# Optimization experiments

Measured on AMD Instinct MI355X. Metric: run time of the kernel, lower is better.

Reference implementation:

```python
import jax, jax.numpy as jnp
import numpy as np

R, B, F, C, NCLS = 32, 4096, 256, 4, 1000  # n_rules, batch, n_fea, n_channel, n_cls
K, PAD, POOL = 5, 1, 2                     # kernel_size, padding, pooling_size


def setup_inputs() -> dict:
    key = jax.random.key(0)
    ks = jax.random.split(key, 12)
    L0 = F + 2 * PAD - K + 1          # 254 after conv1
    L1 = L0 // POOL                   # 127 after avgpool1
    L2 = (L1 + 2 * PAD - K + 1) // POOL  # 62 after conv2+avgpool2
    att = C * L2                      # 248 (matches torch att_size formula)
    hid = att // 2                    # 124
    s = lambda k, shape: jax.random.normal(k, shape, dtype=jnp.float32) * 0.05
    return dict(
        data=jax.random.normal(ks[0], (B, F), dtype=jnp.float32),
        proto=s(ks[1], (R, F)),
        conv1_w=s(ks[2], (C, 1, K)), conv1_b=s(ks[3], (C,)),
        conv2_w=s(ks[4], (C, C, K)), conv2_b=s(ks[5], (C,)),
        fc1_w=s(ks[6], (att, hid)), fc1_b=s(ks[7], (hid,)),
        fc2_w=s(ks[8], (hid, 1)), fc2_b=s(ks[9], (1,)),
        consq_w=s(ks[10], (R, F, NCLS)), consq_b=s(ks[11], (R, NCLS)),
        is_train=0,
    )


def _conv1d(x, w, b):
    # x: [N, Cin, L], w: [Cout, Cin, K]
    out = jax.lax.conv_general_dilated(
        x, w, window_strides=(1,), padding=[(PAD, PAD)],
        dimension_numbers=('NCH', 'OIH', 'NCH'))
    return out + b[None, :, None]


def _avgpool2(x):
    # non-overlapping AvgPool1d(2), drops trailing remainder like torch
    L2 = x.shape[-1] // POOL
    return x[..., :L2 * POOL].reshape(x.shape[0], x.shape[1], L2, POOL).mean(-1)


def reference(data, proto, conv1_w, conv1_b, conv2_w, conv2_b,
              fc1_w, fc1_b, fc2_w, fc2_b, consq_w, consq_b, is_train):
    n_batch = data.shape[0]
    # data_diff: [R, B, F] -> shared gating net, fold rules into batch
    diff = (data[None, :, :] - proto[:, None, :]).reshape(R * n_batch, 1, F)
    h = _avgpool2(jax.nn.relu(_conv1d(diff, conv1_w, conv1_b)))
    h = _avgpool2(jax.nn.relu(_conv1d(h, conv2_w, conv2_b)))
    h = h.reshape(R * n_batch, -1)                       # [R*B, att]
    h = jax.nn.relu(h @ fc1_w + fc1_b)                   # [R*B, hid]
    fs_ini = jnp.tanh(h @ fc2_w + fc2_b)                 # [R*B, 1]
    fs_ini = fs_ini.reshape(R, n_batch).T                # cat(dim=1) -> [B, R]
    fs = jax.nn.softmax(fs_ini, axis=1)                  # softmax over rules
    # per-rule experts: grouped matmul [B,F] x [R,F,NCLS]
    expert = jnp.einsum('bf,rfc->rbc', data, consq_w) + consq_b[:, None, :]
    return jnp.einsum('br,rbc->bc', fs, expert)          # [B, NCLS]
```

## Files before the change

kernel.cpp:

```cpp
#include <hip/hip_runtime.h>
#include <hip/hip_bf16.h>

using bf16x8 = __attribute__((ext_vector_type(8))) short;
using f32x4  = __attribute__((ext_vector_type(4))) float;
using v2f    = __attribute__((ext_vector_type(2))) float;

__device__ __forceinline__ unsigned short f2bf_rne(float x) {
    unsigned u = __float_as_uint(x);
    u += 0x7fffu + ((u >> 16) & 1u);
    return (unsigned short)(u >> 16);
}

__device__ __forceinline__ void gload_lds16(const void* g, void* l) {
    __builtin_amdgcn_global_load_lds(
        (const __attribute__((address_space(1))) unsigned int*)g,
        (__attribute__((address_space(3))) unsigned int*)l, 16, 0, 0);
}

constexpr int KP = 8320;
constexpr int KROW = KP * 2;

constexpr size_t OFF_DT  = 0;
constexpr size_t OFF_Q1  = OFF_DT  + (size_t)260 * 4096 * 4;
constexpr size_t OFF_BT  = OFF_Q1  + (size_t)32 * 1024 * 4;
constexpr size_t OFF_C1P = OFF_BT;
constexpr size_t OFF_W1S = OFF_BT  + (size_t)1024 * KP * 2;
constexpr size_t OFF_FSI = OFF_W1S + (size_t)128 * 256 * 2;
constexpr size_t OFF_FS  = OFF_FSI + (size_t)32 * 4096 * 4;
constexpr size_t OFF_ASC = OFF_FS  + (size_t)32 * 4096 * 4;
constexpr size_t OFF_H2  = OFF_ASC;
constexpr size_t OFF_P1  = OFF_ASC + (size_t)4096 * KP * 2;

__global__ __launch_bounds__(256) void k_transpose(const float* __restrict__ data,
                                                   float* __restrict__ dTp) {
    __shared__ float tile[64][65];
    int bx = blockIdx.x & 63;
    int fx = blockIdx.x >> 6;
    int tx = threadIdx.x & 63, ty4 = threadIdx.x >> 6;
#pragma unroll
    for (int i = 0; i < 16; ++i) {
        int ty = ty4 * 16 + i;
        tile[ty][tx] = data[(bx * 64 + ty) * 256 + fx * 64 + tx];
    }
    __syncthreads();
#pragma unroll
    for (int i = 0; i < 16; ++i) {
        int ty = ty4 * 16 + i;
        dTp[(size_t)(fx * 64 + ty + 1) * 4096 + bx * 64 + tx] = tile[tx][ty];
    }
}

__global__ __launch_bounds__(256) void k_zrows(float* __restrict__ dTp) {
    int i = blockIdx.x * 256 + threadIdx.x;
    dTp[i] = 0.f;
    dTp[(size_t)257 * 4096 + i] = 0.f;
}

__global__ __launch_bounds__(256) void k_prep_proto(const float* __restrict__ proto,
                                                    const float* __restrict__ w1,
                                                    const float* __restrict__ b1,
                                                    float* __restrict__ q1p) {
    __shared__ float ps[256];
    __shared__ float w1s[20];
    int r = blockIdx.x, tid = threadIdx.x;
    ps[tid] = proto[r * 256 + tid];
    if (tid < 20) w1s[tid] = w1[tid];
    __syncthreads();
    if (tid < 254) {
#pragma unroll
        for (int c = 0; c < 4; ++c) {
            float s = -b1[c];
#pragma unroll
            for (int k = 0; k < 5; ++k) {
                int x = tid + k - 1;
                float xv = (x >= 0 && x < 256) ? ps[x] : 0.f;
                s += w1s[c * 5 + k] * xv;
            }
            q1p[r * 1024 + c * 256 + tid] = s;
        }
    }
}

__global__ __launch_bounds__(64) void k_prep_c1d(const float* __restrict__ dTp,
                                                 const float* __restrict__ w1,
                                                 float2* __restrict__ c1p) {
    int lane = threadIdx.x;
    int bg = blockIdx.x >> 3, ch = blockIdx.x & 7;
    int l0 = ch << 4;
    int nl = (ch == 7) ? 15 : 16;
    int b = (bg << 6) + lane;
    float w1r[20];
#pragma unroll
    for (int i = 0; i < 20; ++i) w1r[i] = w1[i];
    const float* dp = dTp + (size_t)(2 * l0) * 4096 + b;
    float d[6];
#pragma unroll
    for (int i = 0; i < 6; ++i) d[i] = dp[(size_t)i * 4096];
    dp += (size_t)6 * 4096;
    float2* outp = c1p + b;
    for (int li = 0; li < nl; ++li) {
        int l = l0 + li;
#pragma unroll
        for (int c = 0; c < 4; ++c) {
            float s0 = 0.f, s1 = 0.f;
#pragma unroll
            for (int k = 0; k < 5; ++k) {
                s0 += w1r[c * 5 + k] * d[k];
                s1 += w1r[c * 5 + k] * d[k + 1];
            }
            outp[(size_t)(c * 127 + l) * 4096] = make_float2(s0, s1);
        }
        d[0] = d[2]; d[1] = d[3]; d[2] = d[4]; d[3] = d[5];
        d[4] = dp[0];
        d[5] = dp[4096];
        dp += 8192;
    }
}

__global__ __launch_bounds__(256) void k_castB(const float* __restrict__ cw,
                                               const float* __restrict__ cb,
                                               unsigned short* __restrict__ BT) {
    __shared__ unsigned short L[64 * 137];
    int tid = threadIdx.x;
    int kt = blockIdx.x >> 3, ct = blockIdx.x & 7;
    int k0 = kt << 6, c0 = ct << 7;
#pragma unroll
    for (int i = 0; i < 32; ++i) {
        int flat = i * 256 + tid;
        int cl = flat & 127, kl = flat >> 7;
        int cg = c0 + cl;
        int kg = k0 + kl;
        float v = 0.f;
        if (cg < 1000) {
            if (kg < 8192) v = cw[(size_t)kg * 1000 + cg];
            else if (kg < 8224) v = cb[(size_t)(kg - 8192) * 1000 + cg];
        }
        L[kl * 137 + cl] = f2bf_rne(v);
    }
    __syncthreads();
#pragma unroll
    for (int i = 0; i < 4; ++i) {
        int task = i * 256 + tid;
        int kg = task & 7, cl = task >> 3;
        int base = kg * 8 * 137 + cl;
        unsigned x = (unsigned)L[base] | ((unsigned)L[base + 137] << 16);
        unsigned y = (unsigned)L[base + 2 * 137] | ((unsigned)L[base + 3 * 137] << 16);
        unsigned z = (unsigned)L[base + 4 * 137] | ((unsigned)L[base + 5 * 137] << 16);
        unsigned w = (unsigned)L[base + 6 * 137] | ((unsigned)L[base + 7 * 137] << 16);
        uint4 o; o.x = x; o.y = y; o.z = z; o.w = w;
        int cg = c0 + cl;
        size_t byte = (size_t)cg * KROW + (size_t)(kt << 7) + (size_t)((kg ^ (cg & 7)) << 4);
        *(uint4*)((char*)BT + byte) = o;
    }
}

__global__ __launch_bounds__(256) void k_castW(const float* __restrict__ fc1w,
                                               unsigned short* __restrict__ W1s) {
    int idx = blockIdx.x * 256 + threadIdx.x;
    int col = idx >> 8, k = idx & 255;
    float v = 0.f;
    if (col < 124 && k < 248) {
        int f = (k & 3) * 62 + (k >> 2);
        v = fc1w[f * 124 + col];
    }
    int byte = col * 512 + ((k >> 6) << 7) + ((((k >> 3) & 7) ^ (col & 7)) << 4) + ((k & 7) << 1);
    *(unsigned short*)((char*)W1s + byte) = f2bf_rne(v);
}

__global__ __launch_bounds__(64)
void k_conv2(const float2* __restrict__ c1p,
             const float* __restrict__ q1p,
             const float* __restrict__ w2,
             const float* __restrict__ b2,
             char* __restrict__ h2c) {
    __shared__ unsigned short T[64 * 72];

    int lane = threadIdx.x;
    int job = blockIdx.x;
    int jh = job & 1;
    int bc = (job >> 1) & 63;
    int r  = job >> 7;
    int b0 = bc << 6;
    int b = b0 + lane;
    int rb0 = r * 4096 + b0;
    int j2s = jh ? 32 : 0;
    int j2e = jh ? 62 : 32;

    float w2r[80];
#pragma unroll
    for (int i = 0; i < 80; ++i) w2r[i] = w2[i];
    v2f bb[4];
#pragma unroll
    for (int c = 0; c < 4; ++c) { float t = b2[c]; bb[c][0] = t; bb[c][1] = t; }

    const float* q1row = q1p + r * 1024;
    const float2* cpb = c1p + b;

    auto pooled = [&](int c, int l) -> float {
        float2 v = cpb[(size_t)(c * 127 + l) * 4096];
        float2 q = *(const float2*)(q1row + c * 256 + 2 * l);
        return 0.5f * (fmaxf(v.x - q.x, 0.f) + fmaxf(v.y - q.y, 0.f));
    };

    v2f P[4][5];
#pragma unroll
    for (int c = 0; c < 4; ++c) {
        float pv[6];
#pragma unroll
        for (int idx = 0; idx < 6; ++idx) {
            int l = 2 * j2s - 1 + idx;
            pv[idx] = (l < 0) ? 0.f : pooled(c, l);
        }
#pragma unroll
        for (int k = 0; k < 5; ++k) { P[c][k][0] = pv[k]; P[c][k][1] = pv[k + 1]; }
    }

#pragma unroll 2
    for (int j2 = j2s; j2 < j2e; ++j2) {
        v2f u[4];
#pragma unroll
        for (int c = 0; c < 4; ++c) u[c] = bb[c];
#pragma unroll
        for (int c = 0; c < 4; ++c)
#pragma unroll
            for (int ci = 0; ci < 4; ++ci)
#pragma unroll
                for (int k = 0; k < 5; ++k)
                    u[c] += P[ci][k] * w2r[(c * 4 + ci) * 5 + k];
        {
            float h0 = 0.5f * (fmaxf(u[0][0], 0.f) + fmaxf(u[0][1], 0.f));
            float h1 = 0.5f * (fmaxf(u[1][0], 0.f) + fmaxf(u[1][1], 0.f));
            float h2v = 0.5f * (fmaxf(u[2][0], 0.f) + fmaxf(u[2][1], 0.f));
            float h3 = 0.5f * (fmaxf(u[3][0], 0.f) + fmaxf(u[3][1], 0.f));
            uint2 vv;
            vv.x = (unsigned)f2bf_rne(h0) | ((unsigned)f2bf_rne(h1) << 16);
            vv.y = (unsigned)f2bf_rne(h2v) | ((unsigned)f2bf_rne(h3) << 16);
            *(uint2*)(T + lane * 72 + (j2 & 15) * 4) = vv;
        }
        if (j2 == 61) {
            uint4 z; z.x = z.y = z.z = z.w = 0u;
            *(uint4*)(T + lane * 72 + 56) = z;
        }
        if ((j2 & 15) == 15 || j2 == 61) {
            int chunk = j2 >> 4;
            int g = lane & 7;
#pragma unroll
            for (int i = 0; i < 8; ++i) {
                int sL = i * 8 + (lane >> 3);
                bf16x8 v = *(const bf16x8*)(T + sL * 72 + g * 8);
                int srow = rb0 + sL;
                size_t byte = (size_t)srow * 512 + (size_t)(chunk * 128) + (size_t)((g ^ (srow & 7)) << 4);
                *(bf16x8*)(h2c + byte) = v;
            }
        }
        if (j2 < j2e - 1) {
#pragma unroll
            for (int c = 0; c < 4; ++c) {
                float n0 = pooled(c, 2 * j2 + 5);
                float n1 = pooled(c, 2 * j2 + 6);
                v2f p4v = P[c][4];
                P[c][0] = P[c][2]; P[c][1] = P[c][3]; P[c][2] = p4v;
                v2f t3; t3[0] = p4v[1]; t3[1] = n0;
                v2f t4; t4[0] = n0;     t4[1] = n1;
                P[c][3] = t3; P[c][4] = t4;
            }
        }
    }
}

__global__ __launch_bounds__(256) void k_fc(const char* __restrict__ h2,
                                            const char* __restrict__ W1s,
                                            const float* __restrict__ fc1b,
                                            const float* __restrict__ fc2w,
                                            const float* __restrict__ fc2b,
                                            float* __restrict__ fsiniT) {
    int tid = threadIdx.x, lane = tid & 63, w = tid >> 6;
    int row0 = blockIdx.x * 128 + w * 32;
    int lr = lane & 15, g = lane >> 4, rxor = lr & 7;

    f32x4 acc[2][8] = {};

    const char* arow0 = h2 + (size_t)(row0 + lr) * 512;
    const char* arow1 = arow0 + 16 * 512;

    auto inrowf = [&](int ks) {
        return ((ks >> 1) << 7) + ((((ks * 4 + g) & 7) ^ rxor) << 4);
    };

    bf16x8 a0 = *(const bf16x8*)(arow0 + inrowf(0));
    bf16x8 a1 = *(const bf16x8*)(arow1 + inrowf(0));

#pragma unroll
    for (int ks = 0; ks < 8; ++ks) {
        int ir = inrowf(ks);
        bf16x8 bfr[8];
#pragma unroll
        for (int nf = 0; nf < 8; ++nf)
            bfr[nf] = *(const bf16x8*)(W1s + (nf * 16 + lr) * 512 + ir);
        bf16x8 an0 = a0, an1 = a1;
        if (ks < 7) {
            int ir2 = inrowf(ks + 1);
            an0 = *(const bf16x8*)(arow0 + ir2);
            an1 = *(const bf16x8*)(arow1 + ir2);
        }
#pragma unroll
        for (int nf = 0; nf < 8; ++nf) {
            acc[0][nf] = __builtin_amdgcn_mfma_f32_16x16x32_bf16(a0, bfr[nf], acc[0][nf], 0, 0, 0);
            acc[1][nf] = __builtin_amdgcn_mfma_f32_16x16x32_bf16(a1, bfr[nf], acc[1][nf], 0, 0, 0);
        }
        a0 = an0; a1 = an1;
    }

    float zp[2][4] = {};
#pragma unroll
    for (int nf = 0; nf < 8; ++nf) {
        int col = nf * 16 + lr;
        float b1v = (col < 124) ? fc1b[col] : 0.f;
        float w2v = (col < 124) ? fc2w[col] : 0.f;
#pragma unroll
        for (int mf = 0; mf < 2; ++mf)
#pragma unroll
            for (int q = 0; q < 4; ++q) {
                float h = fmaxf(acc[mf][nf][q] + b1v, 0.f);
                zp[mf][q] += h * w2v;
            }
    }
#pragma unroll
    for (int off = 1; off < 16; off <<= 1) {
#pragma unroll
        for (int mf = 0; mf < 2; ++mf)
#pragma unroll
            for (int q = 0; q < 4; ++q)
                zp[mf][q] += __shfl_xor(zp[mf][q], off, 64);
    }
    if (lr == 0) {
        float c2 = fc2b[0];
#pragma unroll
        for (int mf = 0; mf < 2; ++mf)
#pragma unroll
            for (int q = 0; q < 4; ++q) {
                int srow = row0 + mf * 16 + g * 4 + q;
                fsiniT[srow] = tanhf(zp[mf][q] + c2);
            }
    }
}

__global__ __launch_bounds__(256) void k_softmax(const float* __restrict__ fsiniT,
                                                 float* __restrict__ fsT) {
    int b = blockIdx.x * 256 + threadIdx.x;
    float v[32];
    float m = -1e30f;
#pragma unroll
    for (int r = 0; r < 32; ++r) { v[r] = fsiniT[r * 4096 + b]; m = fmaxf(m, v[r]); }
    float s = 0.f;
#pragma unroll
    for (int r = 0; r < 32; ++r) { v[r] = expf(v[r] - m); s += v[r]; }
    float inv = 1.f / s;
#pragma unroll
    for (int r = 0; r < 32; ++r) fsT[r * 4096 + b] = v[r] * inv;
}

__global__ __launch_bounds__(256) void k_scaleA(const float* __restrict__ data,
                                                const float* __restrict__ fsT,
                                                unsigned short* __restrict__ Asc) {
    int g = blockIdx.x * 256 + threadIdx.x;
    int b = g / 1040, kg = g - b * 1040;
    uint4 o;
    unsigned* op = (unsigned*)&o;
    if (kg < 1024) {
        int r = kg >> 5, f0 = (kg & 31) << 3;
        float fs = fsT[r * 4096 + b];
        const float4* dp = (const float4*)(data + b * 256 + f0);
        float4 v0 = dp[0], v1 = dp[1];
        float vals[8] = {v0.x, v0.y, v0.z, v0.w, v1.x, v1.y, v1.z, v1.w};
#pragma unroll
        for (int i = 0; i < 4; ++i) {
            unsigned lo = f2bf_rne(vals[2 * i] * fs);
            unsigned hi = f2bf_rne(vals[2 * i + 1] * fs);
            op[i] = lo | (hi << 16);
        }
    } else {
        int base = (kg - 1024) << 3;
        op[0] = op[1] = op[2] = op[3] = 0u;
        if (base < 32) {
#pragma unroll
            for (int i = 0; i < 4; ++i) {
                unsigned lo = f2bf_rne(fsT[(base + 2 * i) * 4096 + b]);
                unsigned hi = f2bf_rne(fsT[(base + 2 * i + 1) * 4096 + b]);
                op[i] = lo | (hi << 16);
            }
        }
    }
    size_t byte = (size_t)b * KROW + (size_t)((kg & ~7) << 4) + (size_t)(((kg & 7) ^ (b & 7)) << 4);
    *(uint4*)((char*)Asc + byte) = o;
}

__global__ __launch_bounds__(512) void k_gemm(const unsigned short* __restrict__ Asc,
                                              const unsigned short* __restrict__ BT,
                                              float* __restrict__ out,
                                              _Float16* __restrict__ part1) {
    __shared__ unsigned short As[2][8192];
    __shared__ unsigned short Bs[2][8192];
    int tid = threadIdx.x, lane = tid & 63, w = tid >> 6;
    int wm = w >> 2, wn = w & 3;
    int bid = blockIdx.x;
    int xcd = bid & 7, idx = bid >> 3;
    int mt = (xcd << 2) | (idx >> 4);
    int nt = (idx >> 1) & 7;
    int ks = idx & 1;
    int row0 = mt << 7, col0 = nt << 7;

    f32x4 acc[4][2] = {};

    const char* Ab = (const char*)Asc + (size_t)ks * (KP);
    const char* Bb = (const char*)BT + (size_t)ks * (KP);
    int flat0 = tid * 16, flat1 = tid * 16 + 8192;
    int rowl0 = flat0 >> 7, colB0 = flat0 & 127;
    int rowl1 = flat1 >> 7, colB1 = flat1 & 127;
    const char* aSrc0 = Ab + (size_t)(row0 + rowl0) * KROW + colB0;
    const char* aSrc1 = Ab + (size_t)(row0 + rowl1) * KROW + colB1;
    const char* bSrc0 = Bb + (size_t)(col0 + rowl0) * KROW + colB0;
    const char* bSrc1 = Bb + (size_t)(col0 + rowl1) * KROW + colB1;

    auto stage = [&](int buf, int kt) {
        int off = kt << 7;
        gload_lds16(aSrc0 + off, (char*)&As[buf][0] + flat0);
        gload_lds16(aSrc1 + off, (char*)&As[buf][0] + flat1);
        gload_lds16(bSrc0 + off, (char*)&Bs[buf][0] + flat0);
        gload_lds16(bSrc1 + off, (char*)&Bs[buf][0] + flat1);
    };

    auto compute = [&](int buf) {
        const char* Asb = (const char*)&As[buf][0];
        const char* Bsb = (const char*)&Bs[buf][0];
#pragma unroll
        for (int s = 0; s < 2; ++s) {
            bf16x8 af[4], bfv[2];
            int colByte = ((s << 5) + ((lane >> 4) << 3)) << 1;
#pragma unroll
            for (int mi = 0; mi < 4; ++mi) {
                int rowA = (wm << 6) + (mi << 4) + (lane & 15);
                int byte = (rowA << 7) + colByte;
                af[mi] = *(const bf16x8*)(Asb + (byte ^ ((rowA & 7) << 4)));
            }
#pragma unroll
            for (int ni = 0; ni < 2; ++ni) {
                int rowB = (wn << 5) + (ni << 4) + (lane & 15);
                int byte = (rowB << 7) + colByte;
                bfv[ni] = *(const bf16x8*)(Bsb + (byte ^ ((rowB & 7) << 4)));
            }
#pragma unroll
            for (int mi = 0; mi < 4; ++mi)
#pragma unroll
                for (int ni = 0; ni < 2; ++ni)
                    acc[mi][ni] = __builtin_amdgcn_mfma_f32_16x16x32_bf16(af[mi], bfv[ni], acc[mi][ni], 0, 0, 0);
        }
    };

    stage(0, 0);
    asm volatile("s_waitcnt vmcnt(0)" ::: "memory");
    __syncthreads();
#pragma unroll 1
    for (int kt = 0; kt < 64; ++kt) {
        stage((kt + 1) & 1, kt + 1);
        compute(kt & 1);
        asm volatile("s_waitcnt vmcnt(0)" ::: "memory");
        __syncthreads();
    }
    compute(0);

    int cA = col0 + (wn << 5) + (lane & 15);
    int cB2 = cA + 16;
    int rbase = row0 + (wm << 6) + ((lane >> 4) << 2);

    if (ks == 0) {
#pragma unroll
        for (int mi = 0; mi < 4; ++mi)
#pragma unroll
            for (int q = 0; q < 4; ++q) {
                int row = rbase + mi * 16 + q;
                if (cA < 1000) out[row * 1000 + cA] = acc[mi][0][q];
                if (cB2 < 1000) out[row * 1000 + cB2] = acc[mi][1][q];
            }
    } else {
#pragma unroll
        for (int mi = 0; mi < 4; ++mi)
#pragma unroll
            for (int q = 0; q < 4; ++q) {
                int row = rbase + mi * 16 + q;
                if (cA < 1000) part1[row * 1000 + cA] = (_Float16)acc[mi][0][q];
                if (cB2 < 1000) part1[row * 1000 + cB2] = (_Float16)acc[mi][1][q];
            }
    }
}

__global__ __launch_bounds__(256) void k_reduce(float* __restrict__ out,
                                                const _Float16* __restrict__ p1) {
    int i = (blockIdx.x * 256 + threadIdx.x) * 4;
    float4 o = *(float4*)(out + i);
    o.x += (float)p1[i];
    o.y += (float)p1[i + 1];
    o.z += (float)p1[i + 2];
    o.w += (float)p1[i + 3];
    *(float4*)(out + i) = o;
}

extern "C" void kernel_launch(void* const* d_in, const int* in_sizes, int n_in,
                              void* d_out, int out_size, void* d_ws, size_t ws_size,
                              hipStream_t stream) {
    const float* data  = (const float*)d_in[0];
    const float* proto = (const float*)d_in[1];
    const float* w1    = (const float*)d_in[2];
    const float* b1    = (const float*)d_in[3];
    const float* w2    = (const float*)d_in[4];
    const float* b2    = (const float*)d_in[5];
    const float* fc1w  = (const float*)d_in[6];
    const float* fc1b  = (const float*)d_in[7];
    const float* fc2w  = (const float*)d_in[8];
    const float* fc2b  = (const float*)d_in[9];
    const float* cw    = (const float*)d_in[10];
    const float* cbias = (const float*)d_in[11];
    float* out = (float*)d_out;
    char* ws = (char*)d_ws;

    float* dTp             = (float*)(ws + OFF_DT);
    float* q1p             = (float*)(ws + OFF_Q1);
    float2* c1p            = (float2*)(ws + OFF_C1P);
    unsigned short* BT     = (unsigned short*)(ws + OFF_BT);
    unsigned short* W1s    = (unsigned short*)(ws + OFF_W1S);
    float* fsiniT          = (float*)(ws + OFF_FSI);
    float* fsT             = (float*)(ws + OFF_FS);
    unsigned short* Asc    = (unsigned short*)(ws + OFF_ASC);
    char* h2c              = (char*)(ws + OFF_H2);
    _Float16* part1        = (_Float16*)(ws + OFF_P1);

    hipLaunchKernelGGL(k_transpose, dim3(256), dim3(256), 0, stream, data, dTp);
    hipLaunchKernelGGL(k_zrows, dim3(16), dim3(256), 0, stream, dTp);
    hipLaunchKernelGGL(k_prep_proto, dim3(32), dim3(256), 0, stream, proto, w1, b1, q1p);
    hipLaunchKernelGGL(k_prep_c1d, dim3(512), dim3(64), 0, stream, dTp, w1, c1p);
    hipLaunchKernelGGL(k_conv2, dim3(4096), dim3(64), 0, stream, c1p, q1p, w2, b2, h2c);
    hipLaunchKernelGGL(k_castB, dim3(1040), dim3(256), 0, stream, cw, cbias, BT);
    hipLaunchKernelGGL(k_castW, dim3(128), dim3(256), 0, stream, fc1w, W1s);
    hipLaunchKernelGGL(k_fc, dim3(1024), dim3(256), 0, stream,
                       h2c, (const char*)W1s, fc1b, fc2w, fc2b, fsiniT);
    hipLaunchKernelGGL(k_softmax, dim3(16), dim3(256), 0, stream, fsiniT, fsT);
    hipLaunchKernelGGL(k_scaleA, dim3(16640), dim3(256), 0, stream, data, fsT, Asc);
    hipLaunchKernelGGL(k_gemm, dim3(512), dim3(512), 0, stream, Asc, BT, out, part1);
    hipLaunchKernelGGL(k_reduce, dim3(4000), dim3(256), 0, stream, out, part1);
}
```

Measured before the change: 260.5 us.

## Restructure conv2 to stage pooled conv1 output in LDS and compute output pairs

The conv2 kernel now uses 256-thread blocks. Each block first computes the pooled conv1 activations for 64 samples across all positions and writes them as packed bf16 pairs into shared memory, then syncs. Each wave then computes two pooled outputs per iteration from LDS and writes a whole 16-byte swizzled chunk straight to global memory, replacing the per-lane register sliding window and the LDS transpose staging. This spreads the pooled-input loads across four waves and makes the global stores wider, at the cost of a large shared-memory footprint (about 66 KB per block), which limits occupancy. The intermediate activations are also rounded to bf16 before conv2.

```diff
diff --git a/kernel.cpp b/kernel.cpp
--- a/kernel.cpp
+++ b/kernel.cpp
@@ -167,34 +167,22 @@
     *(unsigned short*)((char*)W1s + byte) = f2bf_rne(v);
 }
 
-__global__ __launch_bounds__(64)
-void k_conv2(const float2* __restrict__ c1p,
-             const float* __restrict__ q1p,
-             const float* __restrict__ w2,
-             const float* __restrict__ b2,
-             char* __restrict__ h2c) {
-    __shared__ unsigned short T[64 * 72];
-
-    int lane = threadIdx.x;
+__global__ __launch_bounds__(256) void k_conv2(const float2* __restrict__ c1p,
+                                               const float* __restrict__ q1p,
+                                               const float* __restrict__ w2,
+                                               const float* __restrict__ b2,
+                                               char* __restrict__ h2c) {
+    __shared__ unsigned Lu[64 * 257];
+
+    int tid = threadIdx.x;
+    int w = tid >> 6, s = tid & 63;
     int job = blockIdx.x;
-    int jh = job & 1;
-    int bc = (job >> 1) & 63;
-    int r  = job >> 7;
-    int b0 = bc << 6;
-    int b = b0 + lane;
-    int rb0 = r * 4096 + b0;
-    int j2s = jh ? 32 : 0;
-    int j2e = jh ? 62 : 32;
-
-    float w2r[80];
-#pragma unroll
-    for (int i = 0; i < 80; ++i) w2r[i] = w2[i];
-    v2f bb[4];
-#pragma unroll
-    for (int c = 0; c < 4; ++c) { float t = b2[c]; bb[c][0] = t; bb[c][1] = t; }
+    int r  = job >> 6;
+    int b0 = (job & 63) << 6;
+    int srow = r * 4096 + b0 + s;
 
     const float* q1row = q1p + r * 1024;
-    const float2* cpb = c1p + b;
+    const float2* cpb = c1p + b0 + s;
 
     auto pooled = [&](int c, int l) -> float {
         float2 v = cpb[(size_t)(c * 127 + l) * 4096];
@@ -202,69 +190,71 @@
         return 0.5f * (fmaxf(v.x - q.x, 0.f) + fmaxf(v.y - q.y, 0.f));
     };
 
-    v2f P[4][5];
-#pragma unroll
-    for (int c = 0; c < 4; ++c) {
-        float pv[6];
-#pragma unroll
-        for (int idx = 0; idx < 6; ++idx) {
-            int l = 2 * j2s - 1 + idx;
-            pv[idx] = (l < 0) ? 0.f : pooled(c, l);
-        }
-#pragma unroll
-        for (int k = 0; k < 5; ++k) { P[c][k][0] = pv[k]; P[c][k][1] = pv[k + 1]; }
-    }
-
-#pragma unroll 2
-    for (int j2 = j2s; j2 < j2e; ++j2) {
-        v2f u[4];
-#pragma unroll
-        for (int c = 0; c < 4; ++c) u[c] = bb[c];
+    {
+        int d0 = w << 4;
+        for (int d = d0; d < d0 + 16; ++d) {
+#pragma unroll
+            for (int c = 0; c < 4; ++c) {
+                float lo = (d > 0) ? pooled(c, 2 * d - 1) : 0.f;
+                float hi = pooled(c, 2 * d);
+                Lu[s * 257 + c * 64 + d] =
+                    (unsigned)f2bf_rne(lo) | ((unsigned)f2bf_rne(hi) << 16);
+            }
+        }
+    }
+    __syncthreads();
+
+    float w2r[80];
+#pragma unroll
+    for (int i = 0; i < 80; ++i) w2r[i] = w2[i];
+    v2f bb[4];
+#pragma unroll
+    for (int c = 0; c < 4; ++c) { float t = b2[c]; bb[c][0] = t; bb[c][1] = t; }
+
+    int p0 = w << 3;
+    int pend = (w == 3) ? 31 : (p0 + 8);
+    const unsigned* Ls = Lu + s * 257;
+    for (int p = p0; p < pend; ++p) {
+        float pv[4][8];
+#pragma unroll
+        for (int c = 0; c < 4; ++c) {
+#pragma unroll
+            for (int e = 0; e < 4; ++e) {
+                unsigned u = Ls[c * 64 + 2 * p + e];
+                pv[c][2 * e]     = __uint_as_float(u << 16);
+                pv[c][2 * e + 1] = __uint_as_float(u & 0xffff0000u);
+            }
+        }
+        v2f ua[4], ub[4];
+#pragma unroll
+        for (int c = 0; c < 4; ++c) { ua[c] = bb[c]; ub[c] = bb[c]; }
 #pragma unroll
         for (int c = 0; c < 4; ++c)
 #pragma unroll
             for (int ci = 0; ci < 4; ++ci)
 #pragma unroll
-                for (int k = 0; k < 5; ++k)
-                    u[c] += P[ci][k] * w2r[(c * 4 + ci) * 5 + k];
-        {
-            float h0 = 0.5f * (fmaxf(u[0][0], 0.f) + fmaxf(u[0][1], 0.f));
-            float h1 = 0.5f * (fmaxf(u[1][0], 0.f) + fmaxf(u[1][1], 0.f));
-            float h2v = 0.5f * (fmaxf(u[2][0], 0.f) + fmaxf(u[2][1], 0.f));
-            float h3 = 0.5f * (fmaxf(u[3][0], 0.f) + fmaxf(u[3][1], 0.f));
-            uint2 vv;
-            vv.x = (unsigned)f2bf_rne(h0) | ((unsigned)f2bf_rne(h1) << 16);
-            vv.y = (unsigned)f2bf_rne(h2v) | ((unsigned)f2bf_rne(h3) << 16);
-            *(uint2*)(T + lane * 72 + (j2 & 15) * 4) = vv;
-        }
-        if (j2 == 61) {
-            uint4 z; z.x = z.y = z.z = z.w = 0u;
-            *(uint4*)(T + lane * 72 + 56) = z;
-        }
-        if ((j2 & 15) == 15 || j2 == 61) {
-            int chunk = j2 >> 4;
-            int g = lane & 7;
-#pragma unroll
-            for (int i = 0; i < 8; ++i) {
-                int sL = i * 8 + (lane >> 3);
-                bf16x8 v = *(const bf16x8*)(T + sL * 72 + g * 8);
-                int srow = rb0 + sL;
-                size_t byte = (size_t)srow * 512 + (size_t)(chunk * 128) + (size_t)((g ^ (srow & 7)) << 4);
-                *(bf16x8*)(h2c + byte) = v;
-            }
-        }
-        if (j2 < j2e - 1) {
-#pragma unroll
-            for (int c = 0; c < 4; ++c) {
-                float n0 = pooled(c, 2 * j2 + 5);
-                float n1 = pooled(c, 2 * j2 + 6);
-                v2f p4v = P[c][4];
-                P[c][0] = P[c][2]; P[c][1] = P[c][3]; P[c][2] = p4v;
-                v2f t3; t3[0] = p4v[1]; t3[1] = n0;
-                v2f t4; t4[0] = n0;     t4[1] = n1;
-                P[c][3] = t3; P[c][4] = t4;
-            }
-        }
+                for (int k = 0; k < 5; ++k) {
+                    float wv = w2r[(c * 4 + ci) * 5 + k];
+                    v2f pa; pa[0] = pv[ci][k];     pa[1] = pv[ci][k + 1];
+                    v2f pb; pb[0] = pv[ci][k + 2]; pb[1] = pv[ci][k + 3];
+                    ua[c] += pa * wv;
+                    ub[c] += pb * wv;
+                }
+        unsigned short hh[8] __attribute__((aligned(16)));
+#pragma unroll
+        for (int c = 0; c < 4; ++c) {
+            hh[c]     = f2bf_rne(0.5f * (fmaxf(ua[c][0], 0.f) + fmaxf(ua[c][1], 0.f)));
+            hh[4 + c] = f2bf_rne(0.5f * (fmaxf(ub[c][0], 0.f) + fmaxf(ub[c][1], 0.f)));
+        }
+        size_t byte = (size_t)srow * 512 + (size_t)((p >> 3) << 7)
+                    + (size_t)(((p & 7) ^ (srow & 7)) << 4);
+        *(bf16x8*)(h2c + byte) = *(bf16x8*)hh;
+    }
+    if (w == 3) {
+        uint4 z; z.x = z.y = z.z = z.w = 0u;
+        size_t byte = (size_t)srow * 512 + (size_t)(3 << 7)
+                    + (size_t)((7 ^ (srow & 7)) << 4);
+        *(uint4*)(h2c + byte) = z;
     }
 }
 
@@ -538,7 +528,7 @@
     hipLaunchKernelGGL(k_zrows, dim3(16), dim3(256), 0, stream, dTp);
     hipLaunchKernelGGL(k_prep_proto, dim3(32), dim3(256), 0, stream, proto, w1, b1, q1p);
     hipLaunchKernelGGL(k_prep_c1d, dim3(512), dim3(64), 0, stream, dTp, w1, c1p);
-    hipLaunchKernelGGL(k_conv2, dim3(4096), dim3(64), 0, stream, c1p, q1p, w2, b2, h2c);
+    hipLaunchKernelGGL(k_conv2, dim3(2048), dim3(256), 0, stream, c1p, q1p, w2, b2, h2c);
     hipLaunchKernelGGL(k_castB, dim3(1040), dim3(256), 0, stream, cw, cbias, BT);
     hipLaunchKernelGGL(k_castW, dim3(128), dim3(256), 0, stream, fc1w, W1s);
     hipLaunchKernelGGL(k_fc, dim3(1024), dim3(256), 0, stream,
```

Measured after the change: 335.9 us. +29.0%, slower.
